# Kernel tuning notes

Measured on AMD Instinct MI355X. Metric: run time of the kernel, lower is better.

## Reference

```python
import jax, jax.numpy as jnp
import numpy as np

EPS = 1e-8  # F.cosine_similarity default eps


def setup_inputs() -> dict:
    key = jax.random.key(0)
    k1, k2, k3 = jax.random.split(key, 3)
    C, S, Q, D_IN, Z_DIM = 256, 5, 64, 1024, 128
    xs = jax.random.normal(k1, (C, S, D_IN), dtype=jnp.float32)
    xq = jax.random.normal(k2, (C, Q, D_IN), dtype=jnp.float32)
    W = jax.random.normal(k3, (D_IN, Z_DIM), dtype=jnp.float32) / np.sqrt(D_IN)
    return {"xs": xs, "xq": xq, "W": W}


def _protonet_loss(xs, xq, W):
    C, S, D = xs.shape
    Q = xq.shape[1]
    # encoder (linear) applied to concatenated support+query, as in the original
    x = jnp.concatenate([xs.reshape(C * S, D), xq.reshape(C * Q, D)], axis=0)
    z = x @ W                                   # [C*(S+Q), Zd]
    Zd = z.shape[-1]
    z_proto = z[: C * S].reshape(C, S, Zd).mean(axis=1)   # [C, Zd]
    zq = z[C * S:]                                        # [C*Q, Zd]
    # squared euclidean distance (GEMM form, avoids [CQ, C, Zd] intermediate)
    d2 = (jnp.sum(zq * zq, axis=-1, keepdims=True)
          + jnp.sum(z_proto * z_proto, axis=-1)[None, :]
          - 2.0 * (zq @ z_proto.T))                       # [C*Q, C]
    lp = d2.reshape(C, Q, C)                              # label_predicts
    # leave-one-out: for each class i drop column i -> [C, Q, C-1]
    loo_idx = np.stack([np.delete(np.arange(C), i) for i in range(C)])  # [C, C-1]
    idx = jnp.broadcast_to(jnp.asarray(loo_idx)[:, None, :], (C, Q, C - 1))
    loo = jnp.take_along_axis(lp, idx, axis=2)            # [C, Q, C-1]
    # pairwise cosine similarity between query rows j<k, per class
    nrm = jnp.maximum(jnp.linalg.norm(loo, axis=-1), EPS)
    a = loo / nrm[..., None]
    sim = jnp.einsum('cqd,ckd->cqk', a, a)                # [C, Q, Q]
    pair_mask = jnp.triu(jnp.ones((Q, Q), dtype=bool), 1)
    n_pairs = C * (Q * (Q - 1) // 2)
    cos_loss = jnp.sum(jnp.where(pair_mask[None], sim, 0.0)) / n_pairs
    # log_softmax over prototype axis; accuracy vs diagonal targets
    log_p_y = jax.nn.log_softmax(-d2, axis=1).reshape(C, Q, C)
    y_hat = jnp.argmax(log_p_y, axis=2)                   # [C, Q]
    acc = jnp.mean((y_hat == jnp.arange(C)[:, None]).astype(jnp.float32))
    # original overwrites loss_val with the cosine-similarity loss
    return cos_loss, acc


def reference(xs, xq, W):
    return _protonet_loss(xs, xq, W)
```

## Files before the change

### kernel.cpp

```cpp
#include <hip/hip_runtime.h>
#include <stdint.h>


typedef __attribute__((ext_vector_type(8))) short s8v;
typedef __attribute__((ext_vector_type(4))) float f32x4;

__device__ __forceinline__ short f2bf(float f) {
  union { float f; unsigned u; } v; v.f = f;
  unsigned r = (v.u + 0x7fffu + ((v.u >> 16) & 1u)) >> 16;
  return (short)r;
}

__device__ __forceinline__ void async16(const void* g, void* s) {
  typedef __attribute__((address_space(3))) uint32_t lds_t;
  typedef const __attribute__((address_space(1))) uint32_t glb_t;
  __builtin_amdgcn_global_load_lds((glb_t*)(uintptr_t)g,
                                   (lds_t*)(uint32_t)(uintptr_t)s, 16, 0, 0);
}

__global__ __launch_bounds__(256) void k_prep(
    const float* __restrict__ xs, const float* __restrict__ W,
    float* __restrict__ xbar, unsigned short* __restrict__ Wt,
    float* __restrict__ n2, float* __restrict__ out) {
  __shared__ unsigned short T[128 * 68];
  const int tid = threadIdx.x;
  if (blockIdx.x < 256) {
    const int c = blockIdx.x;
    if (c == 0 && tid < 2) out[tid] = 0.0f;
    if (tid < 65) n2[c * 65 + tid] = 0.0f;
    const float* b = xs + (size_t)c * 5120;
    for (int e = tid; e < 1024; e += 256) {
      float s = b[e] + b[1024 + e] + b[2048 + e] + b[3072 + e] + b[4096 + e];
      xbar[(size_t)c * 1024 + e] = s * 0.2f;
    }
  } else {
    const int kb = (blockIdx.x - 256) * 64;
#pragma unroll
    for (int s = 0; s < 8; ++s) {
      int idx = tid + s * 256;
      int kr = idx >> 5, n4 = idx & 31;
      float4 v = *(const float4*)(W + (size_t)(kb + kr) * 128 + n4 * 4);
      T[(n4 * 4 + 0) * 68 + kr] = (unsigned short)f2bf(v.x);
      T[(n4 * 4 + 1) * 68 + kr] = (unsigned short)f2bf(v.y);
      T[(n4 * 4 + 2) * 68 + kr] = (unsigned short)f2bf(v.z);
      T[(n4 * 4 + 3) * 68 + kr] = (unsigned short)f2bf(v.w);
    }
    __syncthreads();
#pragma unroll
    for (int s = 0; s < 8; ++s) {
      int idx = tid + s * 256;
      int n = idx >> 4, k4 = idx & 15;
      ushort4 o;
      o.x = T[n * 68 + k4 * 4 + 0];
      o.y = T[n * 68 + k4 * 4 + 1];
      o.z = T[n * 68 + k4 * 4 + 2];
      o.w = T[n * 68 + k4 * 4 + 3];
      *(ushort4*)(Wt + (size_t)n * 1024 + kb + k4 * 4) = o;
    }
  }
}

__global__ __launch_bounds__(256, 2) void k_gemm_z(
    const float* __restrict__ xbar, const float* __restrict__ xq,
    const unsigned short* __restrict__ Wt,
    unsigned short* __restrict__ zb, float* __restrict__ n2) {
  __shared__ __align__(16) char SM[49152];
  const int tid = threadIdx.x;
  const int w = tid >> 6, l = tid & 63, ln = l & 15, qd = l >> 4;
  const int mb = (blockIdx.x >> 1) * 64;
  const int nb = (blockIdx.x & 1) * 64;
  const float* abase = (mb < 256) ? (xbar + (size_t)mb * 1024)
                                  : (xq + (size_t)(mb - 256) * 1024);
  const float* asrc[8];
#pragma unroll
  for (int i = 0; i < 8; ++i) {
    int ar = w * 8 + i;
    int e = ar & 1, ks = (ar >> 1) & 3, rg = ar >> 3;
    asrc[i] = abase + (size_t)(rg * 16 + ln) * 1024 + ks * 32 + qd * 8 + e * 4;
  }
  const unsigned short* bsrc[4];
#pragma unroll
  for (int i = 0; i < 4; ++i) {
    int br = w * 4 + i;
    int ks = br & 3, t = br >> 2;
    bsrc[i] = Wt + (size_t)(nb + t * 16 + ln) * 1024 + ks * 32 + qd * 8;
  }

  f32x4 acc[4] = {};
  for (int kt = 0; kt < 8; ++kt) {
#pragma unroll
    for (int i = 0; i < 8; ++i)
      async16(asrc[i] + kt * 128, SM + (w * 8 + i) * 1024);
#pragma unroll
    for (int i = 0; i < 4; ++i)
      async16(bsrc[i] + kt * 128, SM + 32768 + (w * 4 + i) * 1024);
    __syncthreads();
#pragma unroll
    for (int ks = 0; ks < 4; ++ks) {
      f32x4 alo = *(const f32x4*)(SM + (w * 8 + ks * 2 + 0) * 1024 + l * 16);
      f32x4 ahi = *(const f32x4*)(SM + (w * 8 + ks * 2 + 1) * 1024 + l * 16);
      s8v af = { f2bf(alo[0]), f2bf(alo[1]), f2bf(alo[2]), f2bf(alo[3]),
                 f2bf(ahi[0]), f2bf(ahi[1]), f2bf(ahi[2]), f2bf(ahi[3]) };
#pragma unroll
      for (int t = 0; t < 4; ++t) {
        s8v bf = *(const s8v*)(SM + 32768 + (t * 4 + ks) * 1024 + l * 16);
        acc[t] = __builtin_amdgcn_mfma_f32_16x16x32_bf16(af, bf, acc[t], 0, 0, 0);
      }
    }
    __syncthreads();
  }
#pragma unroll
  for (int p = 0; p < 4; ++p) {
    const int grow = mb + w * 16 + qd * 4 + p;
    float sp = 0.0f;
#pragma unroll
    for (int t = 0; t < 4; ++t) {
      float v = acc[t][p];
      zb[(size_t)grow * 128 + nb + t * 16 + ln] = (unsigned short)f2bf(v);
      sp += v * v;
    }
    sp += __shfl_xor(sp, 1);
    sp += __shfl_xor(sp, 2);
    sp += __shfl_xor(sp, 4);
    sp += __shfl_xor(sp, 8);
    if (ln == 0) atomicAdd(&n2[grow], sp);
  }
}

__global__ __launch_bounds__(256, 1) void k_d2red(
    const unsigned short* __restrict__ zb, const float* __restrict__ n2,
    float* __restrict__ out) {
  __shared__ float Dt[256 * 65];
  __shared__ float rv[256];
  __shared__ int   ri[256];
  __shared__ float rss[256];
  __shared__ float invn[64];
  __shared__ float sred[4];
  __shared__ float s_tc, s_aq2, s_corr;
  const int tid = threadIdx.x;
  const int c = blockIdx.x;
  const int w = tid >> 6, lane = tid & 63, ln = lane & 15, qd = lane >> 4;

  f32x4 acc[16] = {};
  const unsigned short* Az = zb + (size_t)(256 + c * 64 + w * 16 + ln) * 128;
  s8v af[4];
#pragma unroll
  for (int kt = 0; kt < 4; ++kt) af[kt] = *(const s8v*)(Az + kt * 32 + qd * 8);
#pragma unroll
  for (int t = 0; t < 16; ++t) {
    const unsigned short* Bz = zb + (size_t)(t * 16 + ln) * 128 + qd * 8;
    s8v bf0 = *(const s8v*)(Bz + 0 * 32);
    s8v bf1 = *(const s8v*)(Bz + 1 * 32);
    s8v bf2 = *(const s8v*)(Bz + 2 * 32);
    s8v bf3 = *(const s8v*)(Bz + 3 * 32);
    acc[t] = __builtin_amdgcn_mfma_f32_16x16x32_bf16(af[0], bf0, acc[t], 0, 0, 0);
    acc[t] = __builtin_amdgcn_mfma_f32_16x16x32_bf16(af[1], bf1, acc[t], 0, 0, 0);
    acc[t] = __builtin_amdgcn_mfma_f32_16x16x32_bf16(af[2], bf2, acc[t], 0, 0, 0);
    acc[t] = __builtin_amdgcn_mfma_f32_16x16x32_bf16(af[3], bf3, acc[t], 0, 0, 0);
  }
#pragma unroll
  for (int p = 0; p < 4; ++p) {
    int qloc = w * 16 + qd * 4 + p;
    float qn = n2[256 + c * 64 + qloc];
#pragma unroll
    for (int t = 0; t < 16; ++t) {
      int j = t * 16 + ln;
      Dt[j * 65 + qloc] = qn + n2[j] - 2.0f * acc[t][p];
    }
  }
  __syncthreads();

  {
    const int q = tid & 63, jb = (tid >> 6) * 64;
    float mn = 3.4e38f; int mi = 0; float ss = 0.0f;
    for (int jj = 0; jj < 64; ++jj) {
      int j = jb + jj;
      float f = Dt[j * 65 + q];
      ss += f * f;
      if (f < mn) { mn = f; mi = j; }
    }
    rv[tid] = mn; ri[tid] = mi; rss[tid] = ss;
  }
  __syncthreads();
  if (tid < 64) {
    float bm = rv[tid]; int bi = ri[tid]; float ss = rss[tid];
    for (int hh = 1; hh < 4; ++hh) {
      float v = rv[hh * 64 + tid];
      ss += rss[hh * 64 + tid];
      if (v < bm) { bm = v; bi = ri[hh * 64 + tid]; }
    }
    float col = Dt[c * 65 + tid];
    float loo2 = fmaxf(ss - col * col, 0.0f);
    float nrm = fmaxf(sqrtf(loo2), 1e-8f);
    float inv = 1.0f / nrm;
    invn[tid] = inv;
    float aq2 = loo2 * inv * inv;
    float corr = (bi == c) ? 1.0f : 0.0f;
    for (int m = 1; m < 64; m <<= 1) {
      aq2 += __shfl_xor(aq2, m);
      corr += __shfl_xor(corr, m);
    }
    if (tid == 0) { s_aq2 = aq2; s_corr = corr; }
  }
  __syncthreads();
  float t = 0.0f;
  for (int qq = 0; qq < 64; ++qq) t += Dt[tid * 65 + qq] * invn[qq];
  if (tid == c) s_tc = t;
  float t2 = t * t;
  for (int m = 1; m < 64; m <<= 1) t2 += __shfl_xor(t2, m);
  if ((tid & 63) == 0) sred[tid >> 6] = t2;
  __syncthreads();
  if (tid == 0) {
    float S2 = sred[0] + sred[1] + sred[2] + sred[3];
    float bs = 0.5f * (S2 - s_tc * s_tc - s_aq2);
    atomicAdd(&out[0], bs * (1.0f / 516096.0f));
    atomicAdd(&out[1], s_corr * (1.0f / 16384.0f));
  }
}

extern "C" void kernel_launch(void* const* d_in, const int* in_sizes, int n_in,
                              void* d_out, int out_size, void* d_ws, size_t ws_size,
                              hipStream_t stream) {
  const float* xs = (const float*)d_in[0];
  const float* xq = (const float*)d_in[1];
  const float* W  = (const float*)d_in[2];
  float* out = (float*)d_out;

  float* ws = (float*)d_ws;
  float* xbar = ws;
  unsigned short* Wt = (unsigned short*)(xbar + 262144);
  unsigned short* zb = Wt + 131072;
  float* n2 = (float*)(zb + (size_t)16640 * 128);

  k_prep<<<dim3(272), dim3(256), 0, stream>>>(xs, W, xbar, Wt, n2, out);
  k_gemm_z<<<dim3(520), dim3(256), 0, stream>>>(xbar, xq, Wt, zb, n2);
  k_d2red<<<dim3(256), dim3(256), 0, stream>>>(zb, n2, out);
}
```

Before: 147.7 us.

## Double-buffer z GEMM with full-N tiles and direct norm writes

The encoder GEMM now has each block compute the full 128-column output for 64 rows, so the grid shrinks from 520 to 260 blocks and the A operand is read once instead of twice. The K loop uses smaller K steps with two LDS buffers: the next tile's async loads are issued while the current tile is consumed, and one barrier per iteration is dropped. Because each row's norm is now computed by a single block, the atomicAdd into n2 becomes a plain store and the zeroing in k_prep is removed. The trade-off is fewer blocks for the 256 CUs and more accumulator registers per thread.

```diff
diff --git a/kernel.cpp b/kernel.cpp
--- a/kernel.cpp
+++ b/kernel.cpp
@@ -21,13 +21,12 @@
 __global__ __launch_bounds__(256) void k_prep(
     const float* __restrict__ xs, const float* __restrict__ W,
     float* __restrict__ xbar, unsigned short* __restrict__ Wt,
-    float* __restrict__ n2, float* __restrict__ out) {
+    float* __restrict__ out) {
   __shared__ unsigned short T[128 * 68];
   const int tid = threadIdx.x;
   if (blockIdx.x < 256) {
     const int c = blockIdx.x;
     if (c == 0 && tid < 2) out[tid] = 0.0f;
-    if (tid < 65) n2[c * 65 + tid] = 0.0f;
     const float* b = xs + (size_t)c * 5120;
     for (int e = tid; e < 1024; e += 256) {
       float s = b[e] + b[1024 + e] + b[2048 + e] + b[3072 + e] + b[4096 + e];
@@ -64,66 +63,70 @@
     const float* __restrict__ xbar, const float* __restrict__ xq,
     const unsigned short* __restrict__ Wt,
     unsigned short* __restrict__ zb, float* __restrict__ n2) {
-  __shared__ __align__(16) char SM[49152];
+  __shared__ __align__(16) char SM[2][32768];
   const int tid = threadIdx.x;
   const int w = tid >> 6, l = tid & 63, ln = l & 15, qd = l >> 4;
-  const int mb = (blockIdx.x >> 1) * 64;
-  const int nb = (blockIdx.x & 1) * 64;
+  const int mb = blockIdx.x * 64;
   const float* abase = (mb < 256) ? (xbar + (size_t)mb * 1024)
                                   : (xq + (size_t)(mb - 256) * 1024);
-  const float* asrc[8];
-#pragma unroll
-  for (int i = 0; i < 8; ++i) {
-    int ar = w * 8 + i;
-    int e = ar & 1, ks = (ar >> 1) & 3, rg = ar >> 3;
-    asrc[i] = abase + (size_t)(rg * 16 + ln) * 1024 + ks * 32 + qd * 8 + e * 4;
-  }
-  const unsigned short* bsrc[4];
-#pragma unroll
-  for (int i = 0; i < 4; ++i) {
-    int br = w * 4 + i;
-    int ks = br & 3, t = br >> 2;
-    bsrc[i] = Wt + (size_t)(nb + t * 16 + ln) * 1024 + ks * 32 + qd * 8;
-  }
-
-  f32x4 acc[4] = {};
-  for (int kt = 0; kt < 8; ++kt) {
-#pragma unroll
-    for (int i = 0; i < 8; ++i)
-      async16(asrc[i] + kt * 128, SM + (w * 8 + i) * 1024);
-#pragma unroll
-    for (int i = 0; i < 4; ++i)
-      async16(bsrc[i] + kt * 128, SM + 32768 + (w * 4 + i) * 1024);
+  const float* as[4];
+#pragma unroll
+  for (int i = 0; i < 4; ++i)
+    as[i] = abase + (size_t)(w * 16 + ln) * 1024 + (i >> 1) * 32 + qd * 8 + (i & 1) * 4;
+  const unsigned short* bs[4];
+  bs[0] = Wt + (size_t)(2 * w * 16 + ln) * 1024 + qd * 8;
+  bs[1] = bs[0] + 32;
+  bs[2] = bs[0] + 16 * 1024;
+  bs[3] = bs[2] + 32;
+
+  f32x4 acc[8] = {};
+
+#pragma unroll
+  for (int i = 0; i < 4; ++i)
+    async16(as[i], SM[0] + (w * 4 + i) * 1024);
+#pragma unroll
+  for (int i = 0; i < 4; ++i)
+    async16(bs[i], SM[0] + 16384 + (w * 4 + i) * 1024);
+
+  for (int kt = 0; kt < 16; ++kt) {
+    const int buf = kt & 1;
     __syncthreads();
-#pragma unroll
-    for (int ks = 0; ks < 4; ++ks) {
-      f32x4 alo = *(const f32x4*)(SM + (w * 8 + ks * 2 + 0) * 1024 + l * 16);
-      f32x4 ahi = *(const f32x4*)(SM + (w * 8 + ks * 2 + 1) * 1024 + l * 16);
+    if (kt < 15) {
+#pragma unroll
+      for (int i = 0; i < 4; ++i)
+        async16(as[i] + (kt + 1) * 64, SM[buf ^ 1] + (w * 4 + i) * 1024);
+#pragma unroll
+      for (int i = 0; i < 4; ++i)
+        async16(bs[i] + (kt + 1) * 64, SM[buf ^ 1] + 16384 + (w * 4 + i) * 1024);
+    }
+#pragma unroll
+    for (int ks = 0; ks < 2; ++ks) {
+      f32x4 alo = *(const f32x4*)(SM[buf] + (w * 4 + ks * 2 + 0) * 1024 + l * 16);
+      f32x4 ahi = *(const f32x4*)(SM[buf] + (w * 4 + ks * 2 + 1) * 1024 + l * 16);
       s8v af = { f2bf(alo[0]), f2bf(alo[1]), f2bf(alo[2]), f2bf(alo[3]),
                  f2bf(ahi[0]), f2bf(ahi[1]), f2bf(ahi[2]), f2bf(ahi[3]) };
 #pragma unroll
-      for (int t = 0; t < 4; ++t) {
-        s8v bf = *(const s8v*)(SM + 32768 + (t * 4 + ks) * 1024 + l * 16);
+      for (int t = 0; t < 8; ++t) {
+        s8v bf = *(const s8v*)(SM[buf] + 16384 + (t * 2 + ks) * 1024 + l * 16);
         acc[t] = __builtin_amdgcn_mfma_f32_16x16x32_bf16(af, bf, acc[t], 0, 0, 0);
       }
     }
-    __syncthreads();
   }
 #pragma unroll
   for (int p = 0; p < 4; ++p) {
     const int grow = mb + w * 16 + qd * 4 + p;
     float sp = 0.0f;
 #pragma unroll
-    for (int t = 0; t < 4; ++t) {
+    for (int t = 0; t < 8; ++t) {
       float v = acc[t][p];
-      zb[(size_t)grow * 128 + nb + t * 16 + ln] = (unsigned short)f2bf(v);
+      zb[(size_t)grow * 128 + t * 16 + ln] = (unsigned short)f2bf(v);
       sp += v * v;
     }
     sp += __shfl_xor(sp, 1);
     sp += __shfl_xor(sp, 2);
     sp += __shfl_xor(sp, 4);
     sp += __shfl_xor(sp, 8);
-    if (ln == 0) atomicAdd(&n2[grow], sp);
+    if (ln == 0) n2[grow] = sp;
   }
 }
 
@@ -232,7 +235,7 @@
   unsigned short* zb = Wt + 131072;
   float* n2 = (float*)(zb + (size_t)16640 * 128);
 
-  k_prep<<<dim3(272), dim3(256), 0, stream>>>(xs, W, xbar, Wt, n2, out);
-  k_gemm_z<<<dim3(520), dim3(256), 0, stream>>>(xbar, xq, Wt, zb, n2);
+  k_prep<<<dim3(272), dim3(256), 0, stream>>>(xs, W, xbar, Wt, out);
+  k_gemm_z<<<dim3(260), dim3(256), 0, stream>>>(xbar, xq, Wt, zb, n2);
   k_d2red<<<dim3(256), dim3(256), 0, stream>>>(zb, n2, out);
 }
```

After: 139.2 us. 1.06x faster.
